# Optimization experiments

Hardware: AMD Instinct MI355X
Metric: run time of the kernel (lower is better)

## Reference

```python
import jax, jax.numpy as jnp
import numpy as np

DIM = 64
OUT_DIM = 64
CUTOFF = 5.0
N = 2048


def setup_inputs() -> dict:
    key = jax.random.key(0)
    k_atoms, k_w = jax.random.split(key)
    atoms = jax.random.normal(k_atoms, (N, 3), dtype=jnp.float32) * 5.0
    init = jax.nn.initializers.glorot_normal()
    # Original code (buggily) reuses the same key for both inits; we mirror that.
    w1 = init(k_w, (DIM, 4), jnp.float32)
    w2 = init(k_w, (4, OUT_DIM), jnp.float32)
    return {"atoms": atoms, "w1": w1, "w2": w2, "n_atoms": N}


def reference(atoms, w1, w2, n_atoms):
    # f_k = (k+1) * pi, k = 0..dim-1
    f = (jnp.arange(DIM, dtype=jnp.float32) + 1.0) * jnp.pi
    # pairwise distances: (N, N)
    diff = atoms[None, :, :] - atoms[:, None, :]
    x = jnp.linalg.norm(diff, axis=-1)
    x_ext = x[..., None] + 1e-08                     # (N, N, 1)
    # Bessel RBF basis: (N, N, dim)
    basis = jnp.sqrt(2.0 / CUTOFF) * jnp.sin(f * x_ext / CUTOFF) / x_ext
    # tiny projection dim -> 4 -> out_dim; contract small dim first
    w = w1 @ w2                                      # (dim, out_dim)
    return jnp.einsum('ijd,do->ijo', basis, w)
```

## Files before the change

kernel.cpp:

```cpp
#include <hip/hip_runtime.h>
#include <math.h>

#define NATOMS 2048
#define DIM 64

typedef float f32x4 __attribute__((ext_vector_type(4)));


template <int CTRL>
__device__ __forceinline__ float dpp_add(float v) {
    int m = __builtin_amdgcn_update_dpp(0, __float_as_int(v), CTRL, 0xF, 0xF, true);
    return v + __int_as_float(m);
}
__device__ __forceinline__ float swz_add_xor4(float v) {
    return v + __int_as_float(__builtin_amdgcn_ds_swizzle(__float_as_int(v), 0x101F));
}

__global__ __launch_bounds__(256, 4) void bessel_rbf_kernel(
    const float* __restrict__ atoms,
    const float* __restrict__ w1,
    const float* __restrict__ w2,
    float* __restrict__ out)
{
    __shared__ float s_at[NATOMS * 3];

    const int tid  = threadIdx.x;
    const int lane = tid & 63;
    const int waveInBlock = tid >> 6;
    const int q = lane & 7;
    const int g = lane >> 3;
    const int d0 = q * 8;

    {
        const float4* ga = reinterpret_cast<const float4*>(atoms);
        float4* sa = reinterpret_cast<float4*>(s_at);
#pragma unroll
        for (int r = 0; r < 6; ++r)
            sa[tid + 256 * r] = ga[tid + 256 * r];
    }

    float w1r[8][4];
#pragma unroll
    for (int k = 0; k < 8; ++k) {
        float4 v = *reinterpret_cast<const float4*>(w1 + (d0 + k) * 4);
        w1r[k][0] = v.x; w1r[k][1] = v.y; w1r[k][2] = v.z; w1r[k][3] = v.w;
    }
    const float PREF = 0.6324555320336759f;
    float w2a[4][4], w2b[4][4];
#pragma unroll
    for (int m = 0; m < 4; ++m) {
        float4 va = *reinterpret_cast<const float4*>(w2 + m * DIM + 4 * q);
        float4 vb = *reinterpret_cast<const float4*>(w2 + m * DIM + 32 + 4 * q);
        w2a[m][0] = va.x * PREF; w2a[m][1] = va.y * PREF;
        w2a[m][2] = va.z * PREF; w2a[m][3] = va.w * PREF;
        w2b[m][0] = vb.x * PREF; w2b[m][1] = vb.y * PREF;
        w2b[m][2] = vb.z * PREF; w2b[m][3] = vb.w * PREF;
    }

    __syncthreads();

    const unsigned wid = __builtin_amdgcn_readfirstlane(
        (unsigned)blockIdx.x * 4u + (unsigned)waveInBlock);
    const int i       = (int)(wid >> 2);
    const int colBase = (int)(wid & 3u) * 512;

    const float ax = s_at[i * 3 + 0];
    const float ay = s_at[i * 3 + 1];
    const float az = s_at[i * 3 + 2];

    const float dk1 = (float)(d0 + 1);
    f32x4* __restrict__ out4 = reinterpret_cast<f32x4*>(out);
    const size_t rowBase = (size_t)i * 2048 + (size_t)colBase;

#pragma unroll 2
    for (int it = 0; it < 64; ++it) {
        const int j = colBase + it * 8 + g;

        const float bx = s_at[j * 3 + 0];
        const float by = s_at[j * 3 + 1];
        const float bz = s_at[j * 3 + 2];

        const float dx = ax - bx, dy = ay - by, dz = az - bz;
        float x = __builtin_amdgcn_sqrtf(fmaf(dx, dx, fmaf(dy, dy, dz * dz)));
        x += 1e-8f;
        const float inv = __builtin_amdgcn_rcpf(x);
        const float xr  = x * 0.1f;

        float r0 = dk1 * xr;
        float r1 = r0 + xr;
        r0 = r0 - floorf(r0);
        r1 = r1 - floorf(r1);
        float rc = xr - floorf(xr);
        const float a0   = __builtin_amdgcn_sinf(r0) * inv;
        const float a1   = __builtin_amdgcn_sinf(r1) * inv;
        const float c1   = __builtin_amdgcn_cosf(rc);
        const float twoC = c1 + c1;

        float t[4];
#pragma unroll
        for (int m = 0; m < 4; ++m)
            t[m] = fmaf(a1, w1r[1][m], a0 * w1r[0][m]);
        float sp = a0, sc = a1;
#pragma unroll
        for (int k = 2; k < 8; ++k) {
            const float sn = fmaf(twoC, sc, -sp);
#pragma unroll
            for (int m = 0; m < 4; ++m)
                t[m] = fmaf(sn, w1r[k][m], t[m]);
            sp = sc; sc = sn;
        }

#pragma unroll
        for (int m = 0; m < 4; ++m) {
            t[m] = dpp_add<0xB1>(t[m]);
            t[m] = dpp_add<0x4E>(t[m]);
            t[m] = swz_add_xor4(t[m]);
        }

        f32x4 oA, oB;
        oA.x = fmaf(t[0], w2a[0][0], fmaf(t[1], w2a[1][0], fmaf(t[2], w2a[2][0], t[3] * w2a[3][0])));
        oA.y = fmaf(t[0], w2a[0][1], fmaf(t[1], w2a[1][1], fmaf(t[2], w2a[2][1], t[3] * w2a[3][1])));
        oA.z = fmaf(t[0], w2a[0][2], fmaf(t[1], w2a[1][2], fmaf(t[2], w2a[2][2], t[3] * w2a[3][2])));
        oA.w = fmaf(t[0], w2a[0][3], fmaf(t[1], w2a[1][3], fmaf(t[2], w2a[2][3], t[3] * w2a[3][3])));
        oB.x = fmaf(t[0], w2b[0][0], fmaf(t[1], w2b[1][0], fmaf(t[2], w2b[2][0], t[3] * w2b[3][0])));
        oB.y = fmaf(t[0], w2b[0][1], fmaf(t[1], w2b[1][1], fmaf(t[2], w2b[2][1], t[3] * w2b[3][1])));
        oB.z = fmaf(t[0], w2b[0][2], fmaf(t[1], w2b[1][2], fmaf(t[2], w2b[2][2], t[3] * w2b[3][2])));
        oB.w = fmaf(t[0], w2b[0][3], fmaf(t[1], w2b[1][3], fmaf(t[2], w2b[2][3], t[3] * w2b[3][3])));

        const size_t base = (rowBase + (size_t)(it * 8 + g)) * 16;
        out4[base + q]     = oA;
        out4[base + 8 + q] = oB;
    }
}

extern "C" void kernel_launch(void* const* d_in, const int* in_sizes, int n_in,
                              void* d_out, int out_size, void* d_ws, size_t ws_size,
                              hipStream_t stream) {
    const float* atoms = (const float*)d_in[0];
    const float* w1    = (const float*)d_in[1];
    const float* w2    = (const float*)d_in[2];
    float* out         = (float*)d_out;

    dim3 grid(2048), block(256);
    hipLaunchKernelGGL(bessel_rbf_kernel, grid, block, 0, stream, atoms, w1, w2, out);
}
```

Before: 197.0 us.

## Exploit pairwise-distance symmetry: compute upper triangle and write mirrored tiles

Each wave now works on a pair of rows (i and 2047-i) for load balance and evaluates only the tiles with j at or above the 8-aligned diagonal. Every result is written both to (i,j) and to (j,i). This roughly halves the sqrt/sin/cos and the projection arithmetic. Total output bytes stay the same, and the mirrored stores hit scattered rows, which could hurt write coalescing in a kernel that already looks close to bandwidth-bound. Tiles near the diagonal are written twice.

```diff
diff --git a/kernel.cpp b/kernel.cpp
--- a/kernel.cpp
+++ b/kernel.cpp
@@ -61,20 +61,21 @@
 
     const unsigned wid = __builtin_amdgcn_readfirstlane(
         (unsigned)blockIdx.x * 4u + (unsigned)waveInBlock);
-    const int i       = (int)(wid >> 2);
-    const int colBase = (int)(wid & 3u) * 512;
+    const int task = (int)(wid >> 3);
+    const int sub  = (int)(wid & 7u);
+    const int iA = task, iB = 2047 - task;
+    const int itersA = 256 - (iA >> 3);
+    const int jA0 = iA & ~7;
+    const int jB0 = iB & ~7;
 
-    const float ax = s_at[i * 3 + 0];
-    const float ay = s_at[i * 3 + 1];
-    const float az = s_at[i * 3 + 2];
+    const float axA = s_at[iA*3+0], ayA = s_at[iA*3+1], azA = s_at[iA*3+2];
+    const float axB = s_at[iB*3+0], ayB = s_at[iB*3+1], azB = s_at[iB*3+2];
 
     const float dk1 = (float)(d0 + 1);
     f32x4* __restrict__ out4 = reinterpret_cast<f32x4*>(out);
-    const size_t rowBase = (size_t)i * 2048 + (size_t)colBase;
 
-#pragma unroll 2
-    for (int it = 0; it < 64; ++it) {
-        const int j = colBase + it * 8 + g;
+    auto body = [&](int i, int j0, float ax, float ay, float az) {
+        const int j = j0 + g;
 
         const float bx = s_at[j * 3 + 0];
         const float by = s_at[j * 3 + 1];
@@ -127,10 +128,21 @@
         oB.z = fmaf(t[0], w2b[0][2], fmaf(t[1], w2b[1][2], fmaf(t[2], w2b[2][2], t[3] * w2b[3][2])));
         oB.w = fmaf(t[0], w2b[0][3], fmaf(t[1], w2b[1][3], fmaf(t[2], w2b[2][3], t[3] * w2b[3][3])));
 
-        const size_t base = (rowBase + (size_t)(it * 8 + g)) * 16;
-        out4[base + q]     = oA;
-        out4[base + 8 + q] = oB;
-    }
+        const unsigned bDir = ((unsigned)i * 2048u + (unsigned)j) * 16u;
+        const unsigned bMir = ((unsigned)j * 2048u + (unsigned)i) * 16u;
+        out4[bDir + q]     = oA;
+        out4[bDir + 8 + q] = oB;
+        out4[bMir + q]     = oA;
+        out4[bMir + 8 + q] = oB;
+    };
+
+    int it = sub;
+#pragma unroll 2
+    for (; it < itersA; it += 8)
+        body(iA, jA0 + it * 8, axA, ayA, azA);
+#pragma unroll 2
+    for (; it < 257; it += 8)
+        body(iB, jB0 + (it - itersA) * 8, axB, ayB, azB);
 }
 
 extern "C" void kernel_launch(void* const* d_in, const int* in_sizes, int n_in,
```

Result: slower. 207.1 us (+5.1%).
